# Kernel optimization log

Measured on AMD Instinct MI355X. Metric: run time of the kernel, lower is better.

Reference implementation:

```python
import jax, jax.numpy as jnp
import numpy as np

NEG_SLOPE = 0.01
LN_EPS = 1e-5

def _layer_norm(h, g, b):
    mu = jnp.mean(h, axis=-1, keepdims=True)
    var = jnp.mean(jnp.square(h - mu), axis=-1, keepdims=True)
    return (h - mu) * jax.lax.rsqrt(var + LN_EPS) * g + b

def _mlp(h, Wa, ba, g, be, Wb, bb):
    h = h @ Wa + ba
    h = jnp.where(h >= 0, h, NEG_SLOPE * h)  # LeakyReLU
    h = _layer_norm(h, g, be)
    return h @ Wb + bb

def setup_inputs() -> dict:
    N, E = 50000, 800000
    DN, DE, DG, DO = 128, 64, 32, 128
    key = jax.random.key(0)
    ks = jax.random.split(key, 16)
    def lin(k, fan_in, fan_out):
        lim = 1.0 / np.sqrt(fan_in)
        k1, k2 = jax.random.split(k)
        W = jax.random.uniform(k1, (fan_in, fan_out), jnp.float32, -lim, lim)
        b = jax.random.uniform(k2, (fan_out,), jnp.float32, -lim, lim)
        return W, b
    W1a, b1a = lin(ks[0], DN + DE + DG, DO)
    W1b, b1b = lin(ks[1], DO, DO)
    W2a, b2a = lin(ks[2], DN + DO, DO)
    W2b, b2b = lin(ks[3], DO, DO)
    return {
        "x": jax.random.normal(ks[4], (N, DN), jnp.float32),
        "edge_index": jax.random.randint(ks[5], (2, E), 0, N, jnp.int32),
        "edge_attr": jax.random.normal(ks[6], (E, DE), jnp.float32),
        "u": jax.random.normal(ks[7], (DG,), jnp.float32),
        "batch": jnp.zeros((N,), jnp.int32),
        "W1a": W1a, "b1a": b1a,
        "g1": jnp.ones((DO,), jnp.float32), "be1": jnp.zeros((DO,), jnp.float32),
        "W1b": W1b, "b1b": b1b,
        "W2a": W2a, "b2a": b2a,
        "g2": jnp.ones((DO,), jnp.float32), "be2": jnp.zeros((DO,), jnp.float32),
        "W2b": W2b, "b2b": b2b,
    }

def reference(x, edge_index, edge_attr, u, batch,
              W1a, b1a, g1, be1, W1b, b1b,
              W2a, b2a, g2, be2, W2b, b2b):
    src, dest = edge_index[0], edge_index[1]
    E = edge_attr.shape[0]
    N = x.shape[0]
    # gather + concat: [E, DN+DE+DG]
    h = jnp.concatenate([x[src], edge_attr,
                         jnp.broadcast_to(u[None, :], (E, u.shape[0]))], axis=1)
    h = _mlp(h, W1a, b1a, g1, be1, W1b, b1b)
    # scatter_mean by dest
    sums = jax.ops.segment_sum(h, dest, num_segments=N)
    cnt = jax.ops.segment_sum(jnp.ones((E,), h.dtype), dest, num_segments=N)
    agg = sums / jnp.maximum(cnt, 1.0)[:, None]
    return _mlp(jnp.concatenate([x, agg], axis=1), W2a, b2a, g2, be2, W2b, b2b)
```

## Files before the change

kernel.cpp:

```cpp
#include <hip/hip_runtime.h>
#include <hip/hip_bf16.h>

constexpr int DN = 128, DE = 64, DG = 32, DO = 128;
constexpr int K1 = DN + DE + DG;
constexpr int K2 = DN + DO;
constexpr float NEG_SLOPE = 0.01f;
constexpr float LN_EPS = 1e-5f;

constexpr int EPB = 128;
constexpr int NPB = 8;
constexpr int A_LD = 40;

typedef __attribute__((ext_vector_type(8))) short bf16x8;
typedef __attribute__((ext_vector_type(4))) float f32x4;

__device__ inline unsigned short f2bf(float f) {
    unsigned u = __builtin_bit_cast(unsigned, f);
    u += 0x7FFFu + ((u >> 16) & 1u);
    return (unsigned short)(u >> 16);
}

__global__ __launch_bounds__(256) void edge_kernel(
    const float* __restrict__ x, const int* __restrict__ edge_index,
    const float* __restrict__ edge_attr, const float* __restrict__ u,
    const float* __restrict__ W1a,
    const float* __restrict__ b1a, const float* __restrict__ g1,
    const float* __restrict__ be1,
    float* __restrict__ sums, float* __restrict__ cnt, int E)
{
    __shared__ unsigned short s_a[EPB * A_LD];
    __shared__ unsigned short s_b[128 * A_LD];
    __shared__ int s_src[EPB], s_dst[EPB];

    const int tid  = threadIdx.x;
    const int lane = tid & 63, wave = tid >> 6;
    const int l15  = lane & 15, quad = lane >> 4;
    const int ebase  = blockIdx.x * EPB;
    const int evalid = min(EPB, E - ebase);

    if (tid < EPB) {
        int e = ebase + tid;
        bool v = tid < evalid;
        s_src[tid] = v ? edge_index[e] : 0;
        s_dst[tid] = v ? edge_index[E + e] : 0;
    }
    __syncthreads();

    f32x4 acc[2][8];
#pragma unroll
    for (int mt = 0; mt < 2; ++mt)
#pragma unroll
        for (int nt = 0; nt < 8; ++nt) acc[mt][nt] = (f32x4){0.f, 0.f, 0.f, 0.f};

    const int e0 = tid >> 3;
    const int k4 = (tid & 7) * 4;

    for (int ks = 0; ks < 7; ++ks) {
        const int kbase = ks * 32;
#pragma unroll
        for (int it = 0; it < 4; ++it) {
            int e = e0 + it * 32;
            float4 v;
            if (ks < 4) {
                v = *(const float4*)&x[(long)s_src[e] * DN + kbase + k4];
            } else if (ks < 6) {
                long row = min((long)(ebase + e), (long)E - 1);
                v = *(const float4*)&edge_attr[row * DE + (kbase - DN) + k4];
            } else {
                v = *(const float4*)&u[k4];
            }
            ushort4 b;
            b.x = f2bf(v.x); b.y = f2bf(v.y); b.z = f2bf(v.z); b.w = f2bf(v.w);
            *(ushort4*)&s_a[e * A_LD + k4] = b;
        }
#pragma unroll
        for (int it = 0; it < 8; ++it) {
            int p = tid + it * 256;
            int k2 = p >> 7, n = p & 127;
            float w0 = W1a[(long)(kbase + 2 * k2) * DO + n];
            float w1 = W1a[(long)(kbase + 2 * k2 + 1) * DO + n];
            unsigned pk = (unsigned)f2bf(w0) | ((unsigned)f2bf(w1) << 16);
            *(unsigned*)&s_b[n * A_LD + 2 * k2] = pk;
        }
        __syncthreads();
        bf16x8 a0 = *(const bf16x8*)&s_a[(wave * 32 + l15) * A_LD + quad * 8];
        bf16x8 a1 = *(const bf16x8*)&s_a[(wave * 32 + 16 + l15) * A_LD + quad * 8];
#pragma unroll
        for (int nt = 0; nt < 8; ++nt) {
            bf16x8 b = *(const bf16x8*)&s_b[(nt * 16 + l15) * A_LD + quad * 8];
            acc[0][nt] = __builtin_amdgcn_mfma_f32_16x16x32_bf16(a0, b, acc[0][nt], 0, 0, 0);
            acc[1][nt] = __builtin_amdgcn_mfma_f32_16x16x32_bf16(a1, b, acc[1][nt], 0, 0, 0);
        }
        __syncthreads();
    }

    float ba[8], gg[8], bb[8];
#pragma unroll
    for (int nt = 0; nt < 8; ++nt) {
        int col = nt * 16 + l15;
        ba[nt] = b1a[col]; gg[nt] = g1[col]; bb[nt] = be1[col];
    }
#pragma unroll
    for (int mt = 0; mt < 2; ++mt) {
#pragma unroll
        for (int r = 0; r < 4; ++r) {
            float v[8];
            float s = 0.f, q = 0.f;
#pragma unroll
            for (int nt = 0; nt < 8; ++nt) {
                float t = acc[mt][nt][r] + ba[nt];
                t = (t >= 0.f) ? t : NEG_SLOPE * t;
                v[nt] = t; s += t; q += t * t;
            }
#pragma unroll
            for (int off = 1; off < 16; off <<= 1) {
                s += __shfl_xor(s, off, 64);
                q += __shfl_xor(q, off, 64);
            }
            float mu  = s * (1.f / DO);
            float var = q * (1.f / DO) - mu * mu;
            float rs  = rsqrtf(var + LN_EPS);
            int lrow = wave * 32 + mt * 16 + quad * 4 + r;
            if (lrow < evalid) {
                long base = (long)s_dst[lrow] * DO;
#pragma unroll
                for (int nt = 0; nt < 8; ++nt) {
                    float h = (v[nt] - mu) * rs * gg[nt] + bb[nt];
                    atomicAdd(&sums[base + nt * 16 + l15], h);
                }
            }
        }
    }
    if (tid < evalid) atomicAdd(&cnt[s_dst[tid]], 1.0f);
}

__global__ __launch_bounds__(128) void node_kernel(
    const float* __restrict__ x, const float* __restrict__ sums,
    const float* __restrict__ cnt,
    const float* __restrict__ W1b, const float* __restrict__ b1b,
    const float* __restrict__ W2a, const float* __restrict__ b2a,
    const float* __restrict__ g2, const float* __restrict__ be2,
    const float* __restrict__ W2b, const float* __restrict__ b2b,
    float* __restrict__ out, int N)
{
    __shared__ float s_pre[NPB][DO];
    __shared__ float s_in[NPB][K2];
    __shared__ float s_hn[NPB][DO];
    __shared__ float s_red[2][2][NPB];
    __shared__ float s_cflag[NPB];

    const int tid = threadIdx.x;
    const int j = tid;
    const int lane = tid & 63;
    const int wave = tid >> 6;
    const int nbase = blockIdx.x * NPB;
    const int nvalid = min(NPB, N - nbase);

    for (int idx = tid; idx < NPB * DO; idx += 128) {
        int n = idx >> 7, k = idx & 127;
        float v = 0.f, xv = 0.f;
        if (n < nvalid) {
            int node = nbase + n;
            float c = cnt[node];
            if (k == 0) s_cflag[n] = (c > 0.f) ? 1.f : 0.f;
            c = (c > 1.f) ? c : 1.f;
            v  = sums[(long)node * DO + k] / c;
            xv = x[(long)node * DN + k];
        } else if (k == 0) {
            s_cflag[n] = 0.f;
        }
        s_pre[n][k] = v;
        s_in[n][k]  = xv;
    }
    __syncthreads();

    {
        float aggv[NPB];
#pragma unroll
        for (int n = 0; n < NPB; n++) aggv[n] = 0.f;
        for (int kk = 0; kk < DO; kk += 4) {
            const float w0 = W1b[(kk + 0) * DO + j];
            const float w1 = W1b[(kk + 1) * DO + j];
            const float w2 = W1b[(kk + 2) * DO + j];
            const float w3 = W1b[(kk + 3) * DO + j];
#pragma unroll
            for (int n = 0; n < NPB; n++) {
                const float4 h = *reinterpret_cast<const float4*>(&s_pre[n][kk]);
                aggv[n] = fmaf(h.x, w0, fmaf(h.y, w1, fmaf(h.z, w2, fmaf(h.w, w3, aggv[n]))));
            }
        }
        const float b1 = b1b[j];
#pragma unroll
        for (int n = 0; n < NPB; n++) s_in[n][DN + j] = aggv[n] + s_cflag[n] * b1;
    }
    __syncthreads();

    float acc[NPB];
#pragma unroll
    for (int n = 0; n < NPB; n++) acc[n] = 0.f;
    for (int kk = 0; kk < K2; kk += 4) {
        const float w0 = W2a[(kk + 0) * DO + j];
        const float w1 = W2a[(kk + 1) * DO + j];
        const float w2 = W2a[(kk + 2) * DO + j];
        const float w3 = W2a[(kk + 3) * DO + j];
#pragma unroll
        for (int n = 0; n < NPB; n++) {
            const float4 h = *reinterpret_cast<const float4*>(&s_in[n][kk]);
            acc[n] = fmaf(h.x, w0, fmaf(h.y, w1, fmaf(h.z, w2, fmaf(h.w, w3, acc[n]))));
        }
    }

    const float ba = b2a[j];
#pragma unroll
    for (int n = 0; n < NPB; n++) {
        float v = acc[n] + ba;
        acc[n] = (v >= 0.f) ? v : NEG_SLOPE * v;
    }

#pragma unroll
    for (int n = 0; n < NPB; n++) {
        float s = acc[n], s2 = acc[n] * acc[n];
        for (int off = 32; off; off >>= 1) {
            s += __shfl_down(s, off, 64);
            s2 += __shfl_down(s2, off, 64);
        }
        if (lane == 0) { s_red[wave][0][n] = s; s_red[wave][1][n] = s2; }
    }
    __syncthreads();

    const float g = g2[j], be = be2[j];
#pragma unroll
    for (int n = 0; n < NPB; n++) {
        float sum = s_red[0][0][n] + s_red[1][0][n];
        float sq  = s_red[0][1][n] + s_red[1][1][n];
        float mu = sum * (1.f / DO);
        float var = sq * (1.f / DO) - mu * mu;
        float rs = rsqrtf(var + LN_EPS);
        s_hn[n][j] = (acc[n] - mu) * rs * g + be;
    }
    __syncthreads();

    float acc2[NPB];
#pragma unroll
    for (int n = 0; n < NPB; n++) acc2[n] = 0.f;
    for (int kk = 0; kk < DO; kk += 4) {
        const float w0 = W2b[(kk + 0) * DO + j];
        const float w1 = W2b[(kk + 1) * DO + j];
        const float w2 = W2b[(kk + 2) * DO + j];
        const float w3 = W2b[(kk + 3) * DO + j];
#pragma unroll
        for (int n = 0; n < NPB; n++) {
            const float4 h = *reinterpret_cast<const float4*>(&s_hn[n][kk]);
            acc2[n] = fmaf(h.x, w0, fmaf(h.y, w1, fmaf(h.z, w2, fmaf(h.w, w3, acc2[n]))));
        }
    }

    const float bb = b2b[j];
#pragma unroll
    for (int n = 0; n < NPB; n++) {
        if (n < nvalid) out[(long)(nbase + n) * DO + j] = acc2[n] + bb;
    }
}

extern "C" void kernel_launch(void* const* d_in, const int* in_sizes, int n_in,
                              void* d_out, int out_size, void* d_ws, size_t ws_size,
                              hipStream_t stream)
{
    const float* x          = (const float*)d_in[0];
    const int*   edge_index = (const int*)d_in[1];
    const float* edge_attr  = (const float*)d_in[2];
    const float* u          = (const float*)d_in[3];
    const float* W1a = (const float*)d_in[5];
    const float* b1a = (const float*)d_in[6];
    const float* g1  = (const float*)d_in[7];
    const float* be1 = (const float*)d_in[8];
    const float* W1b = (const float*)d_in[9];
    const float* b1b = (const float*)d_in[10];
    const float* W2a = (const float*)d_in[11];
    const float* b2a = (const float*)d_in[12];
    const float* g2  = (const float*)d_in[13];
    const float* be2 = (const float*)d_in[14];
    const float* W2b = (const float*)d_in[15];
    const float* b2b = (const float*)d_in[16];

    const int N = in_sizes[0] / DN;
    const int E = in_sizes[2] / DE;
    float* out  = (float*)d_out;

    float* sums = (float*)d_ws;
    float* cnt  = sums + (size_t)N * DO;

    (void)hipMemsetAsync(d_ws, 0, ((size_t)N * DO + N) * sizeof(float), stream);

    const int eblocks = (E + EPB - 1) / EPB;
    edge_kernel<<<eblocks, 256, 0, stream>>>(
        x, edge_index, edge_attr, u, W1a, b1a, g1, be1, sums, cnt, E);

    const int nblocks = (N + NPB - 1) / NPB;
    node_kernel<<<nblocks, 128, 0, stream>>>(
        x, sums, cnt, W1b, b1b, W2a, b2a, g2, be2, W2b, b2b, out, N);
}
```

Before: 833.9 us.

## Use packed half2 atomics for scatter sums and MFMA node MLP

```diff
diff --git a/kernel.cpp b/kernel.cpp
--- a/kernel.cpp
+++ b/kernel.cpp
@@ -1,4 +1,5 @@
 #include <hip/hip_runtime.h>
+#include <hip/hip_fp16.h>
 #include <hip/hip_bf16.h>
 
 constexpr int DN = 128, DE = 64, DG = 32, DO = 128;
@@ -8,8 +9,10 @@
 constexpr float LN_EPS = 1e-5f;
 
 constexpr int EPB = 128;
-constexpr int NPB = 8;
+constexpr int NB  = 64;
 constexpr int A_LD = 40;
+constexpr int B_LD = 40;
+constexpr int H_LD = 264;
 
 typedef __attribute__((ext_vector_type(8))) short bf16x8;
 typedef __attribute__((ext_vector_type(4))) float f32x4;
@@ -26,10 +29,10 @@
     const float* __restrict__ W1a,
     const float* __restrict__ b1a, const float* __restrict__ g1,
     const float* __restrict__ be1,
-    float* __restrict__ sums, float* __restrict__ cnt, int E)
+    __half* __restrict__ sums, float* __restrict__ cnt, int E)
 {
     __shared__ unsigned short s_a[EPB * A_LD];
-    __shared__ unsigned short s_b[128 * A_LD];
+    __shared__ unsigned short s_b[128 * B_LD];
     __shared__ int s_src[EPB], s_dst[EPB];
 
     const int tid  = threadIdx.x;
@@ -80,14 +83,14 @@
             float w0 = W1a[(long)(kbase + 2 * k2) * DO + n];
             float w1 = W1a[(long)(kbase + 2 * k2 + 1) * DO + n];
             unsigned pk = (unsigned)f2bf(w0) | ((unsigned)f2bf(w1) << 16);
-            *(unsigned*)&s_b[n * A_LD + 2 * k2] = pk;
+            *(unsigned*)&s_b[n * B_LD + 2 * k2] = pk;
         }
         __syncthreads();
         bf16x8 a0 = *(const bf16x8*)&s_a[(wave * 32 + l15) * A_LD + quad * 8];
         bf16x8 a1 = *(const bf16x8*)&s_a[(wave * 32 + 16 + l15) * A_LD + quad * 8];
 #pragma unroll
         for (int nt = 0; nt < 8; ++nt) {
-            bf16x8 b = *(const bf16x8*)&s_b[(nt * 16 + l15) * A_LD + quad * 8];
+            bf16x8 b = *(const bf16x8*)&s_b[(nt * 16 + l15) * B_LD + quad * 8];
             acc[0][nt] = __builtin_amdgcn_mfma_f32_16x16x32_bf16(a0, b, acc[0][nt], 0, 0, 0);
             acc[1][nt] = __builtin_amdgcn_mfma_f32_16x16x32_bf16(a1, b, acc[1][nt], 0, 0, 0);
         }
@@ -121,12 +124,16 @@
             float var = q * (1.f / DO) - mu * mu;
             float rs  = rsqrtf(var + LN_EPS);
             int lrow = wave * 32 + mt * 16 + quad * 4 + r;
-            if (lrow < evalid) {
-                long base = (long)s_dst[lrow] * DO;
-#pragma unroll
-                for (int nt = 0; nt < 8; ++nt) {
-                    float h = (v[nt] - mu) * rs * gg[nt] + bb[nt];
-                    atomicAdd(&sums[base + nt * 16 + l15], h);
+            bool doat = (lrow < evalid);
+            long base = (long)s_dst[lrow] * DO;
+#pragma unroll
+            for (int nt = 0; nt < 8; ++nt) {
+                float h  = (v[nt] - mu) * rs * gg[nt] + bb[nt];
+                float hp = __shfl_xor(h, 1, 64);
+                if (doat && ((l15 & 1) == 0)) {
+                    __half2 pv = __halves2half2(__float2half_rn(h),
+                                                __float2half_rn(hp));
+                    unsafeAtomicAdd((__half2*)&sums[base + nt * 16 + l15], pv);
                 }
             }
         }
@@ -134,8 +141,8 @@
     if (tid < evalid) atomicAdd(&cnt[s_dst[tid]], 1.0f);
 }
 
-__global__ __launch_bounds__(128) void node_kernel(
-    const float* __restrict__ x, const float* __restrict__ sums,
+__global__ __launch_bounds__(256) void node_kernel(
+    const float* __restrict__ x, const __half* __restrict__ sums,
     const float* __restrict__ cnt,
     const float* __restrict__ W1b, const float* __restrict__ b1b,
     const float* __restrict__ W2a, const float* __restrict__ b2a,
@@ -143,122 +150,176 @@
     const float* __restrict__ W2b, const float* __restrict__ b2b,
     float* __restrict__ out, int N)
 {
-    __shared__ float s_pre[NPB][DO];
-    __shared__ float s_in[NPB][K2];
-    __shared__ float s_hn[NPB][DO];
-    __shared__ float s_red[2][2][NPB];
-    __shared__ float s_cflag[NPB];
-
-    const int tid = threadIdx.x;
-    const int j = tid;
-    const int lane = tid & 63;
-    const int wave = tid >> 6;
-    const int nbase = blockIdx.x * NPB;
-    const int nvalid = min(NPB, N - nbase);
-
-    for (int idx = tid; idx < NPB * DO; idx += 128) {
-        int n = idx >> 7, k = idx & 127;
-        float v = 0.f, xv = 0.f;
-        if (n < nvalid) {
-            int node = nbase + n;
-            float c = cnt[node];
-            if (k == 0) s_cflag[n] = (c > 0.f) ? 1.f : 0.f;
-            c = (c > 1.f) ? c : 1.f;
-            v  = sums[(long)node * DO + k] / c;
-            xv = x[(long)node * DN + k];
-        } else if (k == 0) {
-            s_cflag[n] = 0.f;
-        }
-        s_pre[n][k] = v;
-        s_in[n][k]  = xv;
+    __shared__ unsigned short s_h[NB * H_LD];
+    __shared__ unsigned short s_b[128 * B_LD];
+    __shared__ float s_cf[NB];
+
+    const int tid  = threadIdx.x;
+    const int lane = tid & 63, wave = tid >> 6;
+    const int l15  = lane & 15, quad = lane >> 4;
+    const int nbase  = blockIdx.x * NB;
+    const int nvalid = min(NB, N - nbase);
+
+#pragma unroll
+    for (int i = 0; i < 8; ++i) {
+        int p = tid + i * 256;
+        int row = p >> 5, c4 = (p & 31) * 4;
+        int node = nbase + min(row, nvalid - 1);
+        float4 v = *(const float4*)&x[(long)node * DN + c4];
+        ushort4 b;
+        b.x = f2bf(v.x); b.y = f2bf(v.y); b.z = f2bf(v.z); b.w = f2bf(v.w);
+        *(ushort4*)&s_h[row * H_LD + c4] = b;
+    }
+#pragma unroll
+    for (int i = 0; i < 8; ++i) {
+        int p = tid + i * 256;
+        int row = p >> 5, c = (p & 31) * 4;
+        int node = nbase + min(row, nvalid - 1);
+        float cn = cnt[node];
+        if (c == 0) s_cf[row] = (cn > 0.f) ? 1.f : 0.f;
+        float inv = 1.f / fmaxf(cn, 1.f);
+        const __half2* sp = (const __half2*)&sums[(long)node * DO + c];
+        float2 a0 = __half22float2(sp[0]);
+        float2 a1 = __half22float2(sp[1]);
+        ushort4 b;
+        b.x = f2bf(a0.x * inv); b.y = f2bf(a0.y * inv);
+        b.z = f2bf(a1.x * inv); b.w = f2bf(a1.y * inv);
+        *(ushort4*)&s_h[row * H_LD + DN + c] = b;
+    }
+
+    const unsigned short* aPtr = &s_h[(wave * 16 + l15) * H_LD];
+
+    f32x4 acc[8];
+
+#pragma unroll
+    for (int nt = 0; nt < 8; ++nt) acc[nt] = (f32x4){0.f, 0.f, 0.f, 0.f};
+    for (int ks = 0; ks < 4; ++ks) {
+        __syncthreads();
+#pragma unroll
+        for (int it = 0; it < 8; ++it) {
+            int p = tid + it * 256;
+            int k2 = p >> 7, n = p & 127;
+            float w0 = W1b[(long)(ks * 32 + 2 * k2) * DO + n];
+            float w1 = W1b[(long)(ks * 32 + 2 * k2 + 1) * DO + n];
+            unsigned pk = (unsigned)f2bf(w0) | ((unsigned)f2bf(w1) << 16);
+            *(unsigned*)&s_b[n * B_LD + 2 * k2] = pk;
+        }
+        __syncthreads();
+        bf16x8 a = *(const bf16x8*)&aPtr[DN + ks * 32 + quad * 8];
+#pragma unroll
+        for (int nt = 0; nt < 8; ++nt) {
+            bf16x8 b = *(const bf16x8*)&s_b[(nt * 16 + l15) * B_LD + quad * 8];
+            acc[nt] = __builtin_amdgcn_mfma_f32_16x16x32_bf16(a, b, acc[nt], 0, 0, 0);
+        }
     }
     __syncthreads();
-
     {
-        float aggv[NPB];
-#pragma unroll
-        for (int n = 0; n < NPB; n++) aggv[n] = 0.f;
-        for (int kk = 0; kk < DO; kk += 4) {
-            const float w0 = W1b[(kk + 0) * DO + j];
-            const float w1 = W1b[(kk + 1) * DO + j];
-            const float w2 = W1b[(kk + 2) * DO + j];
-            const float w3 = W1b[(kk + 3) * DO + j];
-#pragma unroll
-            for (int n = 0; n < NPB; n++) {
-                const float4 h = *reinterpret_cast<const float4*>(&s_pre[n][kk]);
-                aggv[n] = fmaf(h.x, w0, fmaf(h.y, w1, fmaf(h.z, w2, fmaf(h.w, w3, aggv[n]))));
-            }
-        }
-        const float b1 = b1b[j];
-#pragma unroll
-        for (int n = 0; n < NPB; n++) s_in[n][DN + j] = aggv[n] + s_cflag[n] * b1;
+        float b1v[8];
+#pragma unroll
+        for (int nt = 0; nt < 8; ++nt) b1v[nt] = b1b[nt * 16 + l15];
+#pragma unroll
+        for (int reg = 0; reg < 4; ++reg) {
+            int row = wave * 16 + quad * 4 + reg;
+            float cf = s_cf[row];
+#pragma unroll
+            for (int nt = 0; nt < 8; ++nt) {
+                float v = acc[nt][reg] + cf * b1v[nt];
+                s_h[row * H_LD + DN + nt * 16 + l15] = f2bf(v);
+            }
+        }
+    }
+
+#pragma unroll
+    for (int nt = 0; nt < 8; ++nt) acc[nt] = (f32x4){0.f, 0.f, 0.f, 0.f};
+    for (int ks = 0; ks < 8; ++ks) {
+        __syncthreads();
+#pragma unroll
+        for (int it = 0; it < 8; ++it) {
+            int p = tid + it * 256;
+            int k2 = p >> 7, n = p & 127;
+            float w0 = W2a[(long)(ks * 32 + 2 * k2) * DO + n];
+            float w1 = W2a[(long)(ks * 32 + 2 * k2 + 1) * DO + n];
+            unsigned pk = (unsigned)f2bf(w0) | ((unsigned)f2bf(w1) << 16);
+            *(unsigned*)&s_b[n * B_LD + 2 * k2] = pk;
+        }
+        __syncthreads();
+        bf16x8 a = *(const bf16x8*)&aPtr[ks * 32 + quad * 8];
+#pragma unroll
+        for (int nt = 0; nt < 8; ++nt) {
+            bf16x8 b = *(const bf16x8*)&s_b[(nt * 16 + l15) * B_LD + quad * 8];
+            acc[nt] = __builtin_amdgcn_mfma_f32_16x16x32_bf16(a, b, acc[nt], 0, 0, 0);
+        }
     }
     __syncthreads();
-
-    float acc[NPB];
-#pragma unroll
-    for (int n = 0; n < NPB; n++) acc[n] = 0.f;
-    for (int kk = 0; kk < K2; kk += 4) {
-        const float w0 = W2a[(kk + 0) * DO + j];
-        const float w1 = W2a[(kk + 1) * DO + j];
-        const float w2 = W2a[(kk + 2) * DO + j];
-        const float w3 = W2a[(kk + 3) * DO + j];
-#pragma unroll
-        for (int n = 0; n < NPB; n++) {
-            const float4 h = *reinterpret_cast<const float4*>(&s_in[n][kk]);
-            acc[n] = fmaf(h.x, w0, fmaf(h.y, w1, fmaf(h.z, w2, fmaf(h.w, w3, acc[n]))));
-        }
-    }
-
-    const float ba = b2a[j];
-#pragma unroll
-    for (int n = 0; n < NPB; n++) {
-        float v = acc[n] + ba;
-        acc[n] = (v >= 0.f) ? v : NEG_SLOPE * v;
-    }
-
-#pragma unroll
-    for (int n = 0; n < NPB; n++) {
-        float s = acc[n], s2 = acc[n] * acc[n];
-        for (int off = 32; off; off >>= 1) {
-            s += __shfl_down(s, off, 64);
-            s2 += __shfl_down(s2, off, 64);
-        }
-        if (lane == 0) { s_red[wave][0][n] = s; s_red[wave][1][n] = s2; }
-    }
-    __syncthreads();
-
-    const float g = g2[j], be = be2[j];
-#pragma unroll
-    for (int n = 0; n < NPB; n++) {
-        float sum = s_red[0][0][n] + s_red[1][0][n];
-        float sq  = s_red[0][1][n] + s_red[1][1][n];
-        float mu = sum * (1.f / DO);
-        float var = sq * (1.f / DO) - mu * mu;
-        float rs = rsqrtf(var + LN_EPS);
-        s_hn[n][j] = (acc[n] - mu) * rs * g + be;
-    }
-    __syncthreads();
-
-    float acc2[NPB];
-#pragma unroll
-    for (int n = 0; n < NPB; n++) acc2[n] = 0.f;
-    for (int kk = 0; kk < DO; kk += 4) {
-        const float w0 = W2b[(kk + 0) * DO + j];
-        const float w1 = W2b[(kk + 1) * DO + j];
-        const float w2 = W2b[(kk + 2) * DO + j];
-        const float w3 = W2b[(kk + 3) * DO + j];
-#pragma unroll
-        for (int n = 0; n < NPB; n++) {
-            const float4 h = *reinterpret_cast<const float4*>(&s_hn[n][kk]);
-            acc2[n] = fmaf(h.x, w0, fmaf(h.y, w1, fmaf(h.z, w2, fmaf(h.w, w3, acc2[n]))));
-        }
-    }
-
-    const float bb = b2b[j];
-#pragma unroll
-    for (int n = 0; n < NPB; n++) {
-        if (n < nvalid) out[(long)(nbase + n) * DO + j] = acc2[n] + bb;
+    {
+        float ba[8], gg[8], bb[8];
+#pragma unroll
+        for (int nt = 0; nt < 8; ++nt) {
+            int col = nt * 16 + l15;
+            ba[nt] = b2a[col]; gg[nt] = g2[col]; bb[nt] = be2[col];
+        }
+#pragma unroll
+        for (int reg = 0; reg < 4; ++reg) {
+            float v[8];
+            float s = 0.f, q = 0.f;
+#pragma unroll
+            for (int nt = 0; nt < 8; ++nt) {
+                float t = acc[nt][reg] + ba[nt];
+                t = (t >= 0.f) ? t : NEG_SLOPE * t;
+                v[nt] = t; s += t; q += t * t;
+            }
+#pragma unroll
+            for (int off = 1; off < 16; off <<= 1) {
+                s += __shfl_xor(s, off, 64);
+                q += __shfl_xor(q, off, 64);
+            }
+            float mu  = s * (1.f / DO);
+            float var = q * (1.f / DO) - mu * mu;
+            float rs  = rsqrtf(var + LN_EPS);
+            int row = wave * 16 + quad * 4 + reg;
+#pragma unroll
+            for (int nt = 0; nt < 8; ++nt) {
+                float h = (v[nt] - mu) * rs * gg[nt] + bb[nt];
+                s_h[row * H_LD + nt * 16 + l15] = f2bf(h);
+            }
+        }
+    }
+
+#pragma unroll
+    for (int nt = 0; nt < 8; ++nt) acc[nt] = (f32x4){0.f, 0.f, 0.f, 0.f};
+    for (int ks = 0; ks < 4; ++ks) {
+        __syncthreads();
+#pragma unroll
+        for (int it = 0; it < 8; ++it) {
+            int p = tid + it * 256;
+            int k2 = p >> 7, n = p & 127;
+            float w0 = W2b[(long)(ks * 32 + 2 * k2) * DO + n];
+            float w1 = W2b[(long)(ks * 32 + 2 * k2 + 1) * DO + n];
+            unsigned pk = (unsigned)f2bf(w0) | ((unsigned)f2bf(w1) << 16);
+            *(unsigned*)&s_b[n * B_LD + 2 * k2] = pk;
+        }
+        __syncthreads();
+        bf16x8 a = *(const bf16x8*)&aPtr[ks * 32 + quad * 8];
+#pragma unroll
+        for (int nt = 0; nt < 8; ++nt) {
+            bf16x8 b = *(const bf16x8*)&s_b[(nt * 16 + l15) * B_LD + quad * 8];
+            acc[nt] = __builtin_amdgcn_mfma_f32_16x16x32_bf16(a, b, acc[nt], 0, 0, 0);
+        }
+    }
+    {
+        float b2v[8];
+#pragma unroll
+        for (int nt = 0; nt < 8; ++nt) b2v[nt] = b2b[nt * 16 + l15];
+#pragma unroll
+        for (int reg = 0; reg < 4; ++reg) {
+            int row = wave * 16 + quad * 4 + reg;
+            if (row < nvalid) {
+                long base = (long)(nbase + row) * DO;
+#pragma unroll
+                for (int nt = 0; nt < 8; ++nt)
+                    out[base + nt * 16 + l15] = acc[nt][reg] + b2v[nt];
+            }
+        }
     }
 }
 
@@ -287,16 +348,18 @@
     const int E = in_sizes[2] / DE;
     float* out  = (float*)d_out;
 
-    float* sums = (float*)d_ws;
-    float* cnt  = sums + (size_t)N * DO;
-
-    (void)hipMemsetAsync(d_ws, 0, ((size_t)N * DO + N) * sizeof(float), stream);
+    __half* sums = (__half*)d_ws;
+    float*  cnt  = (float*)(sums + (size_t)N * DO);
+
+    (void)hipMemsetAsync(d_ws, 0,
+                         (size_t)N * DO * sizeof(__half) + (size_t)N * sizeof(float),
+                         stream);
 
     const int eblocks = (E + EPB - 1) / EPB;
     edge_kernel<<<eblocks, 256, 0, stream>>>(
         x, edge_index, edge_attr, u, W1a, b1a, g1, be1, sums, cnt, E);
 
-    const int nblocks = (N + NPB - 1) / NPB;
-    node_kernel<<<nblocks, 128, 0, stream>>>(
+    const int nblocks = (N + NB - 1) / NB;
+    node_kernel<<<nblocks, 256, 0, stream>>>(
         x, sums, cnt, W1b, b1b, W2a, b2a, g2, be2, W2b, b2b, out, N);
 }
```

After: 740.8 us. -11.2%, faster.
